# Kernel tuning notes

Measured on AMD Instinct MI355X. Metric: run time of the kernel, lower is better.

The kernel has to match this reference:

```python
import jax, jax.numpy as jnp
import numpy as np

N, M, D, DV = 8192, 8192, 128, 128
N_MASK = 1_000_000


def setup_inputs() -> dict:
    key = jax.random.key(0)
    kq, kk, kv, kr, kc = jax.random.split(key, 5)
    query = jax.random.normal(kq, (N, D), dtype=jnp.float32)
    k = jax.random.normal(kk, (M, D), dtype=jnp.float32)
    value = jax.random.normal(kv, (M, DV), dtype=jnp.float32)
    mask_rows = jax.random.randint(kr, (N_MASK,), 0, N, dtype=jnp.int64 if jax.config.jax_enable_x64 else jnp.int32)
    mask_cols = jax.random.randint(kc, (N_MASK,), 0, M, dtype=jnp.int64 if jax.config.jax_enable_x64 else jnp.int32)
    return {"query": query, "key": k, "value": value,
            "mask_rows": mask_rows, "mask_cols": mask_cols}


def reference(query, key, value, mask_rows, mask_cols):
    d = query.shape[1]
    # [N, M] score matrix: q @ k^T / sqrt(d)
    scores = (query @ key.T) / jnp.sqrt(jnp.asarray(d, dtype=query.dtype))
    # scatter -inf at masked coordinates (torch: scaled[mask[0], mask[1]] = -inf)
    scores = scores.at[mask_rows, mask_cols].set(-jnp.inf)
    attn = jax.nn.softmax(scores, axis=1)
    return attn @ value
```

## Files before the change

kernel.cpp:

```cpp
#include <hip/hip_runtime.h>
#include <stdint.h>

#define NQ 8192
#define NM 8192
#define DD 128
#define DVD 128
#define NQB 64
#define NSPLIT 12

typedef float f32x4 __attribute__((ext_vector_type(4)));
typedef short s16x8 __attribute__((ext_vector_type(8)));
typedef __fp16 fp16x2 __attribute__((ext_vector_type(2)));
union FragU { uint32_t u[4]; s16x8 v; };
union H2U { fp16x2 h; uint32_t u; };

__device__ __forceinline__ uint32_t bf16rne(float x) {
  uint32_t u = __float_as_uint(x);
  return (u + 0x7FFFu + ((u >> 16) & 1u)) >> 16;
}
__device__ __forceinline__ uint32_t pk2(float a, float b) {
  return __builtin_amdgcn_perm(__float_as_uint(b) + 0x8000u,
                               __float_as_uint(a) + 0x8000u, 0x07060302u);
}
__device__ __forceinline__ void glds16(const void* g, void* l) {
  __builtin_amdgcn_global_load_lds((const __attribute__((address_space(1))) uint32_t*)g,
                                   (__attribute__((address_space(3))) uint32_t*)l, 16, 0, 0);
}

#define SZ_MASK ((size_t)(NM / 32) * NQ * 4)
#define OFF_K   (SZ_MASK)
#define SZ_KB   ((size_t)NM * DD * 2)
#define OFF_V   (OFF_K + SZ_KB)
#define OFF_OP  (OFF_V + SZ_KB)
#define SZ_OPH  ((size_t)NQ * DVD * 2)
#define OFF_L   (OFF_OP + (size_t)NSPLIT * SZ_OPH)

__global__ __launch_bounds__(256) void conv_scatter_kernel(
    const float* __restrict__ K, const float* __restrict__ V,
    uint8_t* __restrict__ Kswz, uint8_t* __restrict__ Vtswz,
    const int* __restrict__ mr, const int* __restrict__ mc, int nmask,
    unsigned int* __restrict__ maskT) {
  __shared__ float Vf[32][132];
  int b = blockIdx.x;
  int tid = threadIdx.x;
  if (b < 512) {
    int t = b * 256 + tid;
    int key = t >> 4, c = t & 15;
    const float* s = K + (size_t)key * DD + 8 * c;
    float4 a = *(const float4*)s, bb = *(const float4*)(s + 4);
    uint4 d;
    d.x = bf16rne(a.x) | (bf16rne(a.y) << 16);
    d.y = bf16rne(a.z) | (bf16rne(a.w) << 16);
    d.z = bf16rne(bb.x) | (bf16rne(bb.y) << 16);
    d.w = bf16rne(bb.z) | (bf16rne(bb.w) << 16);
    size_t off = (size_t)(key >> 5) * 8192 + (size_t)(key & 31) * 256 +
                 (size_t)((c ^ (key & 15)) << 4);
    *(uint4*)(Kswz + off) = d;
  } else if (b < 768) {
    int kb = b - 512;
#pragma unroll
    for (int i = 0; i < 4; ++i) {
      int idx = tid + 256 * i;
      int key = idx >> 5, c4 = idx & 31;
      float4 f = *(const float4*)(V + ((size_t)kb * 32 + key) * DVD + 4 * c4);
      *(float4*)&Vf[key][4 * c4] = f;
    }
    __syncthreads();
#pragma unroll
    for (int j = 0; j < 2; ++j) {
      int s = tid + 256 * j;
      int dv = s >> 2, c = s & 3;
      uint4 d;
      uint32_t* dw = (uint32_t*)&d;
#pragma unroll
      for (int w = 0; w < 4; ++w) {
        int k0 = 8 * c + 2 * w;
        dw[w] = bf16rne(Vf[k0][dv]) | (bf16rne(Vf[k0 + 1][dv]) << 16);
      }
      size_t off = (size_t)kb * 8192 + (size_t)dv * 64 + (size_t)((c ^ (dv & 3)) << 4);
      *(uint4*)(Vtswz + off) = d;
    }
  } else {
    size_t i = (size_t)(b - 768) * 256 + tid;
    if (i < (size_t)nmask) {
      int r = mr[i], c = mc[i];
      atomicOr(&maskT[(size_t)(c >> 5) * NQ + r], 1u << (c & 31));
    }
  }
}

__global__ __launch_bounds__(256, 3) void attn_kernel(
    const float* __restrict__ Q, const uint8_t* __restrict__ Kswz,
    const uint8_t* __restrict__ Vtswz, const unsigned int* __restrict__ maskT,
    __fp16* __restrict__ Opart, float* __restrict__ lsum) {
  const int bid = blockIdx.x;
  const int span = bid % NSPLIT;
  const int qblk = bid / NSPLIT;
  const int niter = (span < 4) ? 22 : 21;
  const int kb0 = (span < 4) ? span * 22 : 88 + (span - 4) * 21;

  const int tid = threadIdx.x;
  const int wid = tid >> 6, lane = tid & 63;
  const int g = lane >> 4, qi = lane & 15;
  const int qw = qblk * 128 + wid * 32;

  __shared__ uint8_t smem[36864];
  uint8_t* Klds = smem;
  uint8_t* Vlds = smem + 16384;
  uint32_t* Psc = (uint32_t*)(smem + 32768);

  const float SC = 0.08838834764831845f * 1.4426950408889634f;

  s16x8 qfrag[2][4];
#pragma unroll
  for (int qt = 0; qt < 2; ++qt)
#pragma unroll
    for (int ks = 0; ks < 4; ++ks) {
      const float* qs = Q + (size_t)(qw + 16 * qt + qi) * DD + 32 * ks + 8 * g;
      float4 a = *(const float4*)qs, b = *(const float4*)(qs + 4);
      FragU fu;
      fu.u[0] = bf16rne(a.x * SC) | (bf16rne(a.y * SC) << 16);
      fu.u[1] = bf16rne(a.z * SC) | (bf16rne(a.w * SC) << 16);
      fu.u[2] = bf16rne(b.x * SC) | (bf16rne(b.y * SC) << 16);
      fu.u[3] = bf16rne(b.z * SC) | (bf16rne(b.w * SC) << 16);
      qfrag[qt][ks] = fu.v;
    }

  f32x4 accO[8][2];
#pragma unroll
  for (int dt = 0; dt < 8; ++dt)
#pragma unroll
    for (int qt = 0; qt < 2; ++qt) accO[dt][qt] = (f32x4)0.f;
  f32x4 accL[2] = {(f32x4)0.f, (f32x4)0.f};
  const f32x4 z4 = (f32x4)0.f;

  FragU onesu;
  onesu.u[0] = onesu.u[1] = onesu.u[2] = onesu.u[3] = 0x3F803F80u;
  const s16x8 onesfrag = onesu.v;

  const s16x8* kp0[4];
#pragma unroll
  for (int ks = 0; ks < 4; ++ks)
    kp0[ks] = (const s16x8*)Klds + qi * 16 + ((g + 4 * ks) ^ qi);
  const s16x8* vp0 = (const s16x8*)Vlds + qi * 4 + (g ^ (qi & 3));
  uint32_t* pw = Psc + (wid * 16 + qi) * 16;
  uint32_t* wr[2];
#pragma unroll
  for (int kt = 0; kt < 2; ++kt) wr[kt] = &pw[2 * ((4 * kt + g) ^ (qi & 7))];
  const uint32_t* rd[2];
#pragma unroll
  for (int hb = 0; hb < 2; ++hb) rd[hb] = &pw[2 * ((2 * g + hb) ^ (qi & 7))];

  const uint8_t* ktp = Kswz + (size_t)kb0 * 8192 + (size_t)tid * 16;
  const uint8_t* vtp = Vtswz + (size_t)kb0 * 8192 + (size_t)tid * 16;
  uint8_t* kld = Klds + wid * 1024;
  uint8_t* vld = Vlds + wid * 1024;
  const uint32_t* mq = maskT + (size_t)kb0 * NQ + qw + qi;

  {
    glds16(ktp, kld);
    glds16(ktp + 4096, kld + 4096);
    glds16(vtp, vld);
    glds16(vtp + 4096, vld + 4096);
    ktp += 8192; vtp += 8192;
  }
  uint32_t wmc0 = mq[0], wmc1 = mq[16];
  const uint32_t* mqn = mq + NQ;

  for (int it = 0; it < niter; ++it) {
    __syncthreads();
    const int par = it & 1;
    const int nxt = it + 1 < niter;
    if (nxt) {
      uint8_t* kldn = kld + (par ? 0 : 8192);
      uint8_t* vldn = vld + (par ? 0 : 8192);
      glds16(ktp, kldn);
      glds16(ktp + 4096, kldn + 4096);
      glds16(vtp, vldn);
      glds16(vtp + 4096, vldn + 4096);
      ktp += 8192; vtp += 8192;
    }
    uint32_t wmn0 = mqn[0], wmn1 = mqn[16];
    if (nxt) mqn += NQ;

    const int kofs = par * 512;
    f32x4 sf[2][2];
#pragma unroll
    for (int kt = 0; kt < 2; ++kt) {
      {
        s16x8 kf = kp0[0][kofs + kt * 256];
        sf[0][kt] = __builtin_amdgcn_mfma_f32_16x16x32_bf16(kf, qfrag[0][0], z4, 0, 0, 0);
        sf[1][kt] = __builtin_amdgcn_mfma_f32_16x16x32_bf16(kf, qfrag[1][0], z4, 0, 0, 0);
      }
#pragma unroll
      for (int ks = 1; ks < 4; ++ks) {
        s16x8 kf = kp0[ks][kofs + kt * 256];
        sf[0][kt] = __builtin_amdgcn_mfma_f32_16x16x32_bf16(kf, qfrag[0][ks], sf[0][kt], 0, 0, 0);
        sf[1][kt] = __builtin_amdgcn_mfma_f32_16x16x32_bf16(kf, qfrag[1][ks], sf[1][kt], 0, 0, 0);
      }
    }

    if (__ballot((wmc0 | wmc1) != 0)) {
#pragma unroll
      for (int qt = 0; qt < 2; ++qt) {
        uint32_t wm = qt ? wmc1 : wmc0;
#pragma unroll
        for (int kt = 0; kt < 2; ++kt)
#pragma unroll
          for (int r = 0; r < 4; ++r) {
            int kl = 16 * kt + 4 * g + r;
            if ((wm >> kl) & 1u) sf[qt][kt][r] = -3.0e38f;
          }
      }
    }
    wmc0 = wmn0; wmc1 = wmn1;

    s16x8 pfrag[2];
#pragma unroll
    for (int qt = 0; qt < 2; ++qt) {
#pragma unroll
      for (int kt = 0; kt < 2; ++kt) {
        float p0 = __builtin_amdgcn_exp2f(sf[qt][kt][0]);
        float p1 = __builtin_amdgcn_exp2f(sf[qt][kt][1]);
        float p2 = __builtin_amdgcn_exp2f(sf[qt][kt][2]);
        float p3 = __builtin_amdgcn_exp2f(sf[qt][kt][3]);
        uint2 pk;
        pk.x = pk2(p0, p1);
        pk.y = pk2(p2, p3);
        *(uint2*)wr[kt] = pk;
      }
      uint2 a0 = *(const uint2*)rd[0];
      uint2 b0 = *(const uint2*)rd[1];
      FragU pf;
      pf.u[0] = a0.x; pf.u[1] = a0.y; pf.u[2] = b0.x; pf.u[3] = b0.y;
      pfrag[qt] = pf.v;
    }

    accL[0] = __builtin_amdgcn_mfma_f32_16x16x32_bf16(onesfrag, pfrag[0], accL[0], 0, 0, 0);
    accL[1] = __builtin_amdgcn_mfma_f32_16x16x32_bf16(onesfrag, pfrag[1], accL[1], 0, 0, 0);

#pragma unroll
    for (int dt = 0; dt < 8; ++dt) {
      s16x8 vf = vp0[kofs + dt * 64];
      accO[dt][0] = __builtin_amdgcn_mfma_f32_16x16x32_bf16(vf, pfrag[0], accO[dt][0], 0, 0, 0);
      accO[dt][1] = __builtin_amdgcn_mfma_f32_16x16x32_bf16(vf, pfrag[1], accO[dt][1], 0, 0, 0);
    }
  }

#pragma unroll
  for (int qt = 0; qt < 2; ++qt) {
    int q = qw + 16 * qt + qi;
#pragma unroll
    for (int dt = 0; dt < 8; ++dt) {
      H2U h0, h1;
      h0.h = __builtin_amdgcn_cvt_pkrtz(accO[dt][qt][0], accO[dt][qt][1]);
      h1.h = __builtin_amdgcn_cvt_pkrtz(accO[dt][qt][2], accO[dt][qt][3]);
      uint2 st = {h0.u, h1.u};
      *(uint2*)(Opart + ((size_t)span * NQ + q) * DVD + 16 * dt + 4 * g) = st;
    }
    if (g == 0) lsum[(size_t)span * NQ + q] = accL[qt][0];
  }
}

__global__ __launch_bounds__(256) void merge_kernel(const __fp16* __restrict__ Opart,
                                                    const float* __restrict__ lsum,
                                                    float* __restrict__ out) {
  int idx = blockIdx.x * 256 + threadIdx.x;
  int row = idx >> 5, c4 = idx & 31;
  float den = 0.f;
  f32x4 o = (f32x4)0.f;
#pragma unroll
  for (int p = 0; p < NSPLIT; ++p) {
    den += lsum[(size_t)p * NQ + row];
    uint2 h = *(const uint2*)(Opart + ((size_t)p * NQ + row) * DVD + 4 * c4);
    H2U a, b;
    a.u = h.x; b.u = h.y;
    o[0] += (float)a.h[0]; o[1] += (float)a.h[1];
    o[2] += (float)b.h[0]; o[3] += (float)b.h[1];
  }
  o *= (1.f / den);
  ((f32x4*)out)[idx] = o;
}

extern "C" void kernel_launch(void* const* d_in, const int* in_sizes, int n_in,
                              void* d_out, int out_size, void* d_ws, size_t ws_size,
                              hipStream_t stream) {
  const float* Q = (const float*)d_in[0];
  const float* K = (const float*)d_in[1];
  const float* V = (const float*)d_in[2];
  const int* mr = (const int*)d_in[3];
  const int* mc = (const int*)d_in[4];
  int nmask = in_sizes[3];

  uint8_t* ws = (uint8_t*)d_ws;
  unsigned int* maskT = (unsigned int*)ws;
  uint8_t* Kswz = ws + OFF_K;
  uint8_t* Vtswz = ws + OFF_V;
  __fp16* Opart = (__fp16*)(ws + OFF_OP);
  float* lsum = (float*)(ws + OFF_L);

  hipMemsetAsync(maskT, 0, SZ_MASK, stream);
  conv_scatter_kernel<<<768 + (nmask + 255) / 256, 256, 0, stream>>>(
      K, V, Kswz, Vtswz, mr, mc, nmask, maskT);
  attn_kernel<<<NQB * NSPLIT, 256, 0, stream>>>(Q, Kswz, Vtswz, maskT, Opart, lsum);
  merge_kernel<<<NQ * DVD / 4 / 256, 256, 0, stream>>>(Opart, lsum, (float*)d_out);
}
```

Baseline: 166.7 us.

## Load V fragments directly from global into registers, compute row sums with VALU

V is re-laid out in the prep kernel so that each lane can fetch its MFMA B-fragment straight from global memory. The V tiles are no longer staged through LDS, which halves the LDS footprint and removes the V async copies. The loads are split into two halves issued before and after the QK MFMAs to hide latency. The row-sum MFMA with a ones fragment is replaced by scalar adds of the fp32 probabilities plus cross-lane shuffles at the end. The trade-off is more register pressure and latency exposure, since every wave in a block re-reads the same V data from global or L2.

```diff
diff --git a/kernel.cpp b/kernel.cpp
--- a/kernel.cpp
+++ b/kernel.cpp
@@ -77,7 +77,8 @@
         int k0 = 8 * c + 2 * w;
         dw[w] = bf16rne(Vf[k0][dv]) | (bf16rne(Vf[k0 + 1][dv]) << 16);
       }
-      size_t off = (size_t)kb * 8192 + (size_t)dv * 64 + (size_t)((c ^ (dv & 3)) << 4);
+      size_t off = (size_t)kb * 8192 +
+                   (size_t)(((dv >> 4) * 64) + (c * 16) + (dv & 15)) * 16;
       *(uint4*)(Vtswz + off) = d;
     }
   } else {
@@ -104,10 +105,9 @@
   const int g = lane >> 4, qi = lane & 15;
   const int qw = qblk * 128 + wid * 32;
 
-  __shared__ uint8_t smem[36864];
+  __shared__ uint8_t smem[20480];
   uint8_t* Klds = smem;
-  uint8_t* Vlds = smem + 16384;
-  uint32_t* Psc = (uint32_t*)(smem + 32768);
+  uint32_t* Psc = (uint32_t*)(smem + 16384);
 
   const float SC = 0.08838834764831845f * 1.4426950408889634f;
 
@@ -131,18 +131,13 @@
   for (int dt = 0; dt < 8; ++dt)
 #pragma unroll
     for (int qt = 0; qt < 2; ++qt) accO[dt][qt] = (f32x4)0.f;
-  f32x4 accL[2] = {(f32x4)0.f, (f32x4)0.f};
+  float accL[2] = {0.f, 0.f};
   const f32x4 z4 = (f32x4)0.f;
-
-  FragU onesu;
-  onesu.u[0] = onesu.u[1] = onesu.u[2] = onesu.u[3] = 0x3F803F80u;
-  const s16x8 onesfrag = onesu.v;
 
   const s16x8* kp0[4];
 #pragma unroll
   for (int ks = 0; ks < 4; ++ks)
     kp0[ks] = (const s16x8*)Klds + qi * 16 + ((g + 4 * ks) ^ qi);
-  const s16x8* vp0 = (const s16x8*)Vlds + qi * 4 + (g ^ (qi & 3));
   uint32_t* pw = Psc + (wid * 16 + qi) * 16;
   uint32_t* wr[2];
 #pragma unroll
@@ -152,18 +147,13 @@
   for (int hb = 0; hb < 2; ++hb) rd[hb] = &pw[2 * ((2 * g + hb) ^ (qi & 7))];
 
   const uint8_t* ktp = Kswz + (size_t)kb0 * 8192 + (size_t)tid * 16;
-  const uint8_t* vtp = Vtswz + (size_t)kb0 * 8192 + (size_t)tid * 16;
+  const uint8_t* vtp = Vtswz + (size_t)kb0 * 8192 + (size_t)lane * 16;
   uint8_t* kld = Klds + wid * 1024;
-  uint8_t* vld = Vlds + wid * 1024;
   const uint32_t* mq = maskT + (size_t)kb0 * NQ + qw + qi;
 
-  {
-    glds16(ktp, kld);
-    glds16(ktp + 4096, kld + 4096);
-    glds16(vtp, vld);
-    glds16(vtp + 4096, vld + 4096);
-    ktp += 8192; vtp += 8192;
-  }
+  glds16(ktp, kld);
+  glds16(ktp + 4096, kld + 4096);
+  ktp += 8192;
   uint32_t wmc0 = mq[0], wmc1 = mq[16];
   const uint32_t* mqn = mq + NQ;
 
@@ -171,14 +161,17 @@
     __syncthreads();
     const int par = it & 1;
     const int nxt = it + 1 < niter;
+
+    s16x8 vfrag[8];
+#pragma unroll
+    for (int dt = 0; dt < 4; ++dt)
+      vfrag[dt] = *(const s16x8*)(vtp + dt * 1024);
+
     if (nxt) {
       uint8_t* kldn = kld + (par ? 0 : 8192);
-      uint8_t* vldn = vld + (par ? 0 : 8192);
       glds16(ktp, kldn);
       glds16(ktp + 4096, kldn + 4096);
-      glds16(vtp, vldn);
-      glds16(vtp + 4096, vldn + 4096);
-      ktp += 8192; vtp += 8192;
+      ktp += 8192;
     }
     uint32_t wmn0 = mqn[0], wmn1 = mqn[16];
     if (nxt) mqn += NQ;
@@ -200,6 +193,11 @@
       }
     }
 
+#pragma unroll
+    for (int dt = 4; dt < 8; ++dt)
+      vfrag[dt] = *(const s16x8*)(vtp + dt * 1024);
+    vtp += 8192;
+
     if (__ballot((wmc0 | wmc1) != 0)) {
 #pragma unroll
       for (int qt = 0; qt < 2; ++qt) {
@@ -218,17 +216,20 @@
     s16x8 pfrag[2];
 #pragma unroll
     for (int qt = 0; qt < 2; ++qt) {
+      float ls = 0.f;
 #pragma unroll
       for (int kt = 0; kt < 2; ++kt) {
         float p0 = __builtin_amdgcn_exp2f(sf[qt][kt][0]);
         float p1 = __builtin_amdgcn_exp2f(sf[qt][kt][1]);
         float p2 = __builtin_amdgcn_exp2f(sf[qt][kt][2]);
         float p3 = __builtin_amdgcn_exp2f(sf[qt][kt][3]);
+        ls += (p0 + p1) + (p2 + p3);
         uint2 pk;
         pk.x = pk2(p0, p1);
         pk.y = pk2(p2, p3);
         *(uint2*)wr[kt] = pk;
       }
+      accL[qt] += ls;
       uint2 a0 = *(const uint2*)rd[0];
       uint2 b0 = *(const uint2*)rd[1];
       FragU pf;
@@ -236,15 +237,17 @@
       pfrag[qt] = pf.v;
     }
 
-    accL[0] = __builtin_amdgcn_mfma_f32_16x16x32_bf16(onesfrag, pfrag[0], accL[0], 0, 0, 0);
-    accL[1] = __builtin_amdgcn_mfma_f32_16x16x32_bf16(onesfrag, pfrag[1], accL[1], 0, 0, 0);
-
 #pragma unroll
     for (int dt = 0; dt < 8; ++dt) {
-      s16x8 vf = vp0[kofs + dt * 64];
-      accO[dt][0] = __builtin_amdgcn_mfma_f32_16x16x32_bf16(vf, pfrag[0], accO[dt][0], 0, 0, 0);
-      accO[dt][1] = __builtin_amdgcn_mfma_f32_16x16x32_bf16(vf, pfrag[1], accO[dt][1], 0, 0, 0);
-    }
+      accO[dt][0] = __builtin_amdgcn_mfma_f32_16x16x32_bf16(vfrag[dt], pfrag[0], accO[dt][0], 0, 0, 0);
+      accO[dt][1] = __builtin_amdgcn_mfma_f32_16x16x32_bf16(vfrag[dt], pfrag[1], accO[dt][1], 0, 0, 0);
+    }
+  }
+
+#pragma unroll
+  for (int qt = 0; qt < 2; ++qt) {
+    accL[qt] += __shfl_xor(accL[qt], 16);
+    accL[qt] += __shfl_xor(accL[qt], 32);
   }
 
 #pragma unroll
@@ -258,7 +261,7 @@
       uint2 st = {h0.u, h1.u};
       *(uint2*)(Opart + ((size_t)span * NQ + q) * DVD + 16 * dt + 4 * g) = st;
     }
-    if (g == 0) lsum[(size_t)span * NQ + q] = accL[qt][0];
+    if (g == 0) lsum[(size_t)span * NQ + q] = accL[qt];
   }
 }
 
```

Result: slower. 187.4 us (+12.4%).

## Stage mask words through LDS via async loads and re-lay V tiles

Applied to the files above, without the earlier changes.

Mask bitword reads move from per-lane global loads, prefetched one iteration ahead in registers, to async global-to-LDS copies issued by half a wavefront. They are double-buffered alongside the K and V tiles and read from shared memory each iteration. The transposed-V layout also changes from an XOR swizzle to a linear per-lane layout, so each lane reads V fragments at base+lane. The intent is to cut scattered global loads and register pressure on the mask path. In exchange it uses more LDS and risks bank conflicts on V reads now that the swizzle is gone.

```diff
diff --git a/kernel.cpp b/kernel.cpp
--- a/kernel.cpp
+++ b/kernel.cpp
@@ -77,7 +77,8 @@
         int k0 = 8 * c + 2 * w;
         dw[w] = bf16rne(Vf[k0][dv]) | (bf16rne(Vf[k0 + 1][dv]) << 16);
       }
-      size_t off = (size_t)kb * 8192 + (size_t)dv * 64 + (size_t)((c ^ (dv & 3)) << 4);
+      size_t off = (size_t)kb * 8192 +
+                   (size_t)(((dv >> 4) * 64) + (c * 16) + (dv & 15)) * 16;
       *(uint4*)(Vtswz + off) = d;
     }
   } else {
@@ -104,10 +105,11 @@
   const int g = lane >> 4, qi = lane & 15;
   const int qw = qblk * 128 + wid * 32;
 
-  __shared__ uint8_t smem[36864];
+  __shared__ uint8_t smem[37888];
   uint8_t* Klds = smem;
   uint8_t* Vlds = smem + 16384;
-  uint32_t* Psc = (uint32_t*)(smem + 32768);
+  uint32_t* Mlds = (uint32_t*)(smem + 32768);
+  uint32_t* Psc = (uint32_t*)(smem + 33792);
 
   const float SC = 0.08838834764831845f * 1.4426950408889634f;
 
@@ -142,7 +144,7 @@
 #pragma unroll
   for (int ks = 0; ks < 4; ++ks)
     kp0[ks] = (const s16x8*)Klds + qi * 16 + ((g + 4 * ks) ^ qi);
-  const s16x8* vp0 = (const s16x8*)Vlds + qi * 4 + (g ^ (qi & 3));
+  const s16x8* vp0 = (const s16x8*)Vlds + lane;
   uint32_t* pw = Psc + (wid * 16 + qi) * 16;
   uint32_t* wr[2];
 #pragma unroll
@@ -150,38 +152,40 @@
   const uint32_t* rd[2];
 #pragma unroll
   for (int hb = 0; hb < 2; ++hb) rd[hb] = &pw[2 * ((2 * g + hb) ^ (qi & 7))];
+  const uint32_t* mrd = Mlds + wid * 32 + qi;
 
   const uint8_t* ktp = Kswz + (size_t)kb0 * 8192 + (size_t)tid * 16;
   const uint8_t* vtp = Vtswz + (size_t)kb0 * 8192 + (size_t)tid * 16;
+  const uint8_t* mtp = (const uint8_t*)(maskT + (size_t)kb0 * NQ + qblk * 128) +
+                       (size_t)lane * 16;
   uint8_t* kld = Klds + wid * 1024;
   uint8_t* vld = Vlds + wid * 1024;
-  const uint32_t* mq = maskT + (size_t)kb0 * NQ + qw + qi;
-
-  {
-    glds16(ktp, kld);
-    glds16(ktp + 4096, kld + 4096);
-    glds16(vtp, vld);
-    glds16(vtp + 4096, vld + 4096);
-    ktp += 8192; vtp += 8192;
-  }
-  uint32_t wmc0 = mq[0], wmc1 = mq[16];
-  const uint32_t* mqn = mq + NQ;
+  const bool mstage = (wid == 0) && (lane < 32);
+
+  glds16(ktp, kld);
+  glds16(ktp + 4096, kld + 4096);
+  glds16(vtp, vld);
+  glds16(vtp + 4096, vld + 4096);
+  if (mstage) glds16(mtp, Mlds);
+  ktp += 8192; vtp += 8192; mtp += (size_t)NQ * 4;
 
   for (int it = 0; it < niter; ++it) {
     __syncthreads();
     const int par = it & 1;
     const int nxt = it + 1 < niter;
     if (nxt) {
-      uint8_t* kldn = kld + (par ? 0 : 8192);
-      uint8_t* vldn = vld + (par ? 0 : 8192);
+      uint8_t* kldn = Klds + (par ? 0 : 8192) + wid * 1024;
+      uint8_t* vldn = Vlds + (par ? 0 : 8192) + wid * 1024;
       glds16(ktp, kldn);
       glds16(ktp + 4096, kldn + 4096);
       glds16(vtp, vldn);
       glds16(vtp + 4096, vldn + 4096);
-      ktp += 8192; vtp += 8192;
-    }
-    uint32_t wmn0 = mqn[0], wmn1 = mqn[16];
-    if (nxt) mqn += NQ;
+      if (mstage) glds16(mtp, Mlds + (par ? 0 : 128));
+      ktp += 8192; vtp += 8192; mtp += (size_t)NQ * 4;
+    }
+
+    uint32_t wmc0 = mrd[par * 128];
+    uint32_t wmc1 = mrd[par * 128 + 16];
 
     const int kofs = par * 512;
     f32x4 sf[2][2];
@@ -213,7 +217,6 @@
           }
       }
     }
-    wmc0 = wmn0; wmc1 = wmn1;
 
     s16x8 pfrag[2];
 #pragma unroll
```

Result: no change. 164.2 us (-1.5%).
